# Kernel tuning notes

Hardware: AMD Instinct MI355X
Metric: run time of the kernel (lower is better)

The kernel has to match this reference:

```python
import jax, jax.numpy as jnp
import numpy as np

B, L = 1024, 1024
NCAT, NNUM = 20, 10
CAT_BUCKETS, SEQ_VOCAB = 100000, 50000
E, A, H, QH = 32, 128, 256, 256
TOPK = 30


def _init(key, shape, scale=0.02):
    return scale * jax.random.normal(key, shape, dtype=jnp.float32)


def setup_inputs() -> dict:
    key = jax.random.key(0)
    ks = jax.random.split(key, 24)
    z = lambda *s: jnp.zeros(s, dtype=jnp.float32)
    return {
        "cats": jax.random.randint(ks[0], (B, NCAT), 0, CAT_BUCKETS + 1),
        "nums": jax.random.normal(ks[1], (B, NNUM), dtype=jnp.float32),
        "seqs": jax.random.randint(ks[2], (B, L), 0, SEQ_VOCAB + 1),
        "tgt_ids": jax.random.randint(ks[3], (B,), 0, CAT_BUCKETS + 1),
        "cat_emb": _init(ks[4], (CAT_BUCKETS + 1, E)),
        "seq_emb": _init(ks[5], (SEQ_VOCAB + 1, E)),
        "Wnum": _init(ks[6], (NNUM, E)), "bnum": z(E),
        "Wq": _init(ks[7], (E, A)), "Wk": _init(ks[8], (E, A)), "Wv": _init(ks[9], (E, A)),
        "Wo": _init(ks[10], (A, E)), "bo": z(E),
        "Wpool": _init(ks[11], (NCAT * E, E)), "bpool": z(E),
        "Wmlp": _init(ks[12], (4 * E, H)), "bmlp": z(H),
        "q1_W1": _init(ks[13], (H, QH)), "q1_b1": z(QH),
        "q1_W2": _init(ks[14], (H, QH)), "q1_b2": z(QH),
        "q1_Wp": _init(ks[15], (QH, H)), "q1_bp": z(H),
        "q2_W1": _init(ks[16], (H, QH)), "q2_b1": z(QH),
        "q2_W2": _init(ks[17], (H, QH)), "q2_b2": z(QH),
        "q2_Wp": _init(ks[18], (QH, H)), "q2_bp": z(H),
        "Wout": _init(ks[19], (H, 1)), "bout": z(1),
    }


def _qnn(x, W1, b1, W2, b2, Wp, bp):
    # Quadratic neural block (QIN-style): Hadamard product of two linear maps,
    # projected back with a residual connection. Dropout is identity in eval.
    quad = (x @ W1 + b1) * (x @ W2 + b2)
    return x + quad @ Wp + bp


def reference(cats, nums, seqs, tgt_ids, cat_emb, seq_emb, Wnum, bnum, Wq, Wk, Wv,
              Wo, bo, Wpool, bpool, Wmlp, bmlp,
              q1_W1, q1_b1, q1_W2, q1_b2, q1_Wp, q1_bp,
              q2_W1, q2_b1, q2_W2, q2_b2, q2_Wp, q2_bp, Wout, bout):
    cat_e = cat_emb[cats]                                   # [B, NCAT, E]
    cat_pool = cat_e.reshape(cat_e.shape[0], -1) @ Wpool + bpool   # [B, E]
    num_e = nums @ Wnum + bnum                              # [B, E]
    tgt_e = cat_emb[tgt_ids]                                # [B, E] (tgt_emb shares cat_emb)
    seq_e = seq_emb[seqs]                                   # [B, L, E]

    q = tgt_e @ Wq                                          # [B, A]
    k = seq_e @ Wk                                          # [B, L, A]
    v = seq_e @ Wv                                          # [B, L, A]
    scores = jnp.einsum('ba,bla->bl', q, k) / jnp.sqrt(jnp.float32(A))

    # top-k + scatter mask + masked softmax == softmax over the top-k scores,
    # scattered implicitly via gather of the selected values.
    vals, idx = jax.lax.top_k(scores, TOPK)                 # [B, TOPK]
    w = jax.nn.softmax(vals, axis=1)                        # [B, TOPK]
    v_sel = jnp.take_along_axis(v, idx[:, :, None], axis=1)  # [B, TOPK, A]
    interest = jnp.einsum('bk,bka->ba', w, v_sel) @ Wo + bo  # [B, E]

    fused = jnp.concatenate([tgt_e, interest, cat_pool, num_e], axis=1)  # [B, 4E]
    h = jax.nn.relu(fused @ Wmlp + bmlp)                    # [B, H], dropout=eval
    h = _qnn(h, q1_W1, q1_b1, q1_W2, q1_b2, q1_Wp, q1_bp)
    h = _qnn(h, q2_W1, q2_b1, q2_W2, q2_b2, q2_Wp, q2_bp)
    return (h @ Wout + bout)[:, 0]                          # [B]
```

## Files before the change

kernel.cpp:

```cpp
#include <hip/hip_runtime.h>
#include <hip/hip_fp16.h>

#define B_ 1024
#define L_ 1024
#define NCAT_ 20
#define NNUM_ 10
#define E_ 32
#define A_ 128
#define H_ 256
#define TOPK_ 30
#define INV_SQRT_A 0.08838834764831845f

__device__ __forceinline__ void fma4(float4& a, float s, const float4 w) {
    a.x += s * w.x; a.y += s * w.y; a.z += s * w.z; a.w += s * w.w;
}
__device__ __forceinline__ float4 ldh4(const __half* p) {
    float2 rw = *(const float2*)p;
    const __half2* h = (const __half2*)&rw;
    float2 a = __half22float2(h[0]);
    float2 b = __half22float2(h[1]);
    return make_float4(a.x, a.y, b.x, b.y);
}
__device__ __forceinline__ void ldh24(const __half2* p, float4& w1, float4& w2) {
    float4 rw = *(const float4*)p;
    const __half2* h = (const __half2*)&rw;
    float2 f0 = __half22float2(h[0]), f1 = __half22float2(h[1]);
    float2 f2 = __half22float2(h[2]), f3 = __half22float2(h[3]);
    w1 = make_float4(f0.x, f1.x, f2.x, f3.x);
    w2 = make_float4(f0.y, f1.y, f2.y, f3.y);
}

#define K1_GRID 1356
__global__ __launch_bounds__(256) void fused_prep_kernel(
    const int* __restrict__ cats, const float* __restrict__ nums,
    const int* __restrict__ tgt_ids, const float* __restrict__ cat_emb,
    const float* __restrict__ Wnum, const float* __restrict__ bnum,
    const float* __restrict__ Wq, const float* __restrict__ Wk,
    const float* __restrict__ Wv, const float* __restrict__ Wo,
    const float* __restrict__ Wpool, const float* __restrict__ bpool,
    const float* __restrict__ seq_emb, const float* __restrict__ Wmlp,
    const float* __restrict__ q1W1, const float* __restrict__ q1W2,
    const float* __restrict__ q2W1, const float* __restrict__ q2W2,
    const float* __restrict__ q1Wp, const float* __restrict__ q2Wp,
    float* __restrict__ p_out, float* __restrict__ fused, float* __restrict__ M,
    __half2* __restrict__ seq_h2, __half2* __restrict__ Wmlp_h2,
    __half2* __restrict__ W12_1, __half2* __restrict__ W12_2,
    __half2* __restrict__ Wp1_h2, __half2* __restrict__ Wp2_h2)
{
    const int blk = blockIdx.x;
    const int t = threadIdx.x;

    if (blk < 256) {
        __shared__ float ce[4][NCAT_ * E_];
        __shared__ float tg[4][E_];
        __shared__ float nm[4][NNUM_];
        __shared__ float qs[4][A_];
        __shared__ float part[8][4][E_];
        const int r0 = blk * 4;

        for (int idx = t; idx < 640; idx += 256) {
            const int q = idx >> 3, f4 = idx & 7;
            const int row = q / 20, cat = q % 20;
            const int tok = cats[(r0 + row) * NCAT_ + cat];
            ((float4*)&ce[row][cat * 32])[f4] =
                ((const float4*)(cat_emb + (size_t)tok * 32))[f4];
        }
        if (t < 32) {
            const int row = t >> 3, f4 = t & 7;
            const int tok = tgt_ids[r0 + row];
            ((float4*)&tg[row][0])[f4] =
                ((const float4*)(cat_emb + (size_t)tok * 32))[f4];
        }
        if (t >= 64 && t < 104) {
            const int x = t - 64;
            nm[x / 10][x % 10] = nums[(r0 + x / 10) * NNUM_ + x % 10];
        }
        __syncthreads();

        {
            const int w = t >> 6, lane = t & 63;
            float q0 = 0.f, q1 = 0.f;
#pragma unroll
            for (int e = 0; e < E_; ++e) {
                float te = tg[w][e];
                q0 += te * Wq[e * A_ + lane];
                q1 += te * Wq[e * A_ + lane + 64];
            }
            qs[w][lane] = q0; qs[w][lane + 64] = q1;
        }

        {
            const int iseg = t >> 5;
            const int row = (t >> 3) & 3;
            const int c0 = (t & 7) * 4;
            float4 acc = make_float4(0.f, 0.f, 0.f, 0.f);
            const int i0 = iseg * 80;
            for (int i = i0; i < i0 + 80; ++i) {
                float4 wv = *(const float4*)(Wpool + i * 32 + c0);
                fma4(acc, ce[row][i], wv);
            }
            *(float4*)&part[iseg][row][c0] = acc;
        }
        __syncthreads();

        if (t < 128) {
            const int row = t >> 5, c = t & 31;
            const int b = r0 + row;
            float s = bpool[c];
#pragma unroll
            for (int g = 0; g < 8; ++g) s += part[g][row][c];
            fused[b * 128 + 64 + c] = s;
            fused[b * 128 + c] = tg[row][c];

            float ne = bnum[c];
#pragma unroll
            for (int n = 0; n < NNUM_; ++n) ne += nm[row][n] * Wnum[n * 32 + c];
            fused[b * 128 + 96 + c] = ne;

            float pv = 0.f;
#pragma unroll 8
            for (int a = 0; a < A_; ++a) pv += Wk[c * A_ + a] * qs[row][a];
            p_out[b * 32 + c] = pv;
        }
        return;
    }

    if (blk < 1280) {
        int x = (blk - 256) * 256 + t;
        for (; x < 800016; x += 1024 * 256) {
            float2 v = ((const float2*)seq_emb)[x];
            seq_h2[x] = __float22half2_rn(v);
        }
        return;
    }

    if (blk < 1284) {
        const int o = (blk - 1280) * 256 + t;
        const int j = o >> 5, e = o & 31;
        float sm = 0.f;
#pragma unroll 8
        for (int a = 0; a < A_; ++a) sm += Wv[j * A_ + a] * Wo[a * E_ + e];
        M[o] = sm;
        return;
    }

    if (blk < 1348) {
        int x = (blk - 1284) * 256 + t;
        for (; x < 65536; x += 64 * 256) {
            W12_1[x] = __float22half2_rn(make_float2(q1W1[x], q1W2[x]));
            W12_2[x] = __float22half2_rn(make_float2(q2W1[x], q2W2[x]));
        }
        return;
    }

    {
        int x = (blk - 1348) * 256 + t;
        for (; x < 16384; x += 8 * 256) {
            Wmlp_h2[x] = __float22half2_rn(((const float2*)Wmlp)[x]);
            Wp1_h2[x]  = __float22half2_rn(((const float2*)q1Wp)[x]);
            Wp2_h2[x]  = __float22half2_rn(((const float2*)q2Wp)[x]);
        }
    }
}

__global__ __launch_bounds__(512) void score_topk_kernel(
    const int* __restrict__ seqs, const __half* __restrict__ seq_h,
    const float* __restrict__ seq_emb, const float* __restrict__ p,
    const float* __restrict__ M, const float* __restrict__ bo,
    float* __restrict__ fused)
{
    const int b = blockIdx.x;
    const int t = threadIdx.x;

    __shared__ float sc[L_];
    __shared__ float ps[E_];
    __shared__ float sw[TOPK_];
    __shared__ int   stok[TOPK_];

    if (t < E_) ps[t] = p[b * E_ + t];
    __syncthreads();

    {
        const int tok1 = seqs[b * L_ + t];
        const int tok2 = seqs[b * L_ + t + 512];
        float4 buf[2][4];
        const float4* r1 = (const float4*)(seq_h + (size_t)tok1 * 32);
        const float4* r2 = (const float4*)(seq_h + (size_t)tok2 * 32);
#pragma unroll
        for (int i = 0; i < 4; ++i) buf[0][i] = r1[i];
#pragma unroll
        for (int i = 0; i < 4; ++i) buf[1][i] = r2[i];

        float acc0 = 0.f, acc1 = 0.f;
#pragma unroll
        for (int i = 0; i < 4; ++i) {
            const __half2* h1 = (const __half2*)&buf[0][i];
            const __half2* h2 = (const __half2*)&buf[1][i];
#pragma unroll
            for (int u = 0; u < 4; ++u) {
                float2 f1 = __half22float2(h1[u]);
                float2 f2 = __half22float2(h2[u]);
                acc0 += f1.x * ps[i * 8 + 2 * u] + f1.y * ps[i * 8 + 2 * u + 1];
                acc1 += f2.x * ps[i * 8 + 2 * u] + f2.y * ps[i * 8 + 2 * u + 1];
            }
        }
        sc[t] = acc0 * INV_SQRT_A;
        sc[t + 512] = acc1 * INV_SQRT_A;
    }
    __syncthreads();

    if (t >= 64) return;

    const int lane = t;
    float v[16];
#pragma unroll
    for (int j = 0; j < 16; ++j) v[j] = sc[j * 64 + lane];

    float lmax = v[0]; int lj = 0;
#pragma unroll
    for (int j = 1; j < 16; ++j) if (v[j] > lmax) { lmax = v[j]; lj = j; }

    float myv = -1e30f; int myl = 0;
    for (int k = 0; k < TOPK_; ++k) {
        float best = lmax; int bl = lj * 64 + lane;
#pragma unroll
        for (int off = 32; off > 0; off >>= 1) {
            float ov = __shfl_xor(best, off);
            int   ol = __shfl_xor(bl, off);
            if (ov > best || (ov == best && ol < bl)) { best = ov; bl = ol; }
        }
        if (lane == k) { myv = best; myl = bl; }
        if (lane == (bl & 63)) {
            v[bl >> 6] = -1e30f;
            lmax = v[0]; lj = 0;
#pragma unroll
            for (int j = 1; j < 16; ++j) if (v[j] > lmax) { lmax = v[j]; lj = j; }
        }
    }

    float m = myv;
#pragma unroll
    for (int off = 32; off > 0; off >>= 1) m = fmaxf(m, __shfl_xor(m, off));
    float e = (lane < TOPK_) ? expf(myv - m) : 0.f;
    float s = e;
#pragma unroll
    for (int off = 32; off > 0; off >>= 1) s += __shfl_xor(s, off);
    if (lane < TOPK_) {
        sw[lane]   = e / s;
        stok[lane] = seqs[b * L_ + myl];
    }

    if (lane < E_) {
        float acc = 0.f;
#pragma unroll
        for (int k = 0; k < TOPK_; ++k)
            acc += sw[k] * seq_emb[(size_t)stok[k] * 32 + lane];
        sc[lane] = acc;
    }
    if (lane < E_) {
        float acc = bo[lane];
#pragma unroll
        for (int j = 0; j < E_; ++j) acc += sc[j] * M[j * E_ + lane];
        fused[b * 128 + 32 + lane] = acc;
    }
}

#define RM 4
__global__ __launch_bounds__(512) void mlp_kernel(
    const float* __restrict__ fused,
    const __half* __restrict__ Wmlp_h, const float* __restrict__ bmlp,
    const __half2* __restrict__ W12_1, const float* __restrict__ b11,
    const float* __restrict__ b12, const __half* __restrict__ Wp1_h,
    const float* __restrict__ b1p,
    const __half2* __restrict__ W12_2, const float* __restrict__ b21,
    const float* __restrict__ b22, const __half* __restrict__ Wp2_h,
    const float* __restrict__ b2p,
    const float* __restrict__ Wout, const float* __restrict__ bout,
    float* __restrict__ out)
{
    const int b0 = blockIdx.x * RM;
    const int tid = threadIdx.x;
    const int cg = tid & 63;
    const int iseg = tid >> 6;
    const int c0 = cg * 4;

    __shared__ float xs[RM][128];
    __shared__ float hs[RM][H_];
    __shared__ float ts[RM][H_];
    __shared__ float part[2][8][RM][H_];
    __shared__ float red[8];

    for (int i = tid; i < RM * 128; i += 512) xs[i >> 7][i & 127] = fused[b0 * 128 + i];
    __syncthreads();

    {
        float4 acc[RM];
#pragma unroll
        for (int r = 0; r < RM; ++r) acc[r] = make_float4(0.f, 0.f, 0.f, 0.f);
        const int i0 = iseg * 16;
#pragma unroll
        for (int iq = 0; iq < 4; ++iq) {
            const int i = i0 + iq * 4;
            float4 w[4], xv[RM];
#pragma unroll
            for (int u = 0; u < 4; ++u) w[u] = ldh4(Wmlp_h + (i + u) * H_ + c0);
#pragma unroll
            for (int r = 0; r < RM; ++r) xv[r] = *(const float4*)(&xs[r][i]);
#pragma unroll
            for (int r = 0; r < RM; ++r) {
                fma4(acc[r], xv[r].x, w[0]); fma4(acc[r], xv[r].y, w[1]);
                fma4(acc[r], xv[r].z, w[2]); fma4(acc[r], xv[r].w, w[3]);
            }
        }
#pragma unroll
        for (int r = 0; r < RM; ++r) *(float4*)&part[0][iseg][r][c0] = acc[r];
    }
    __syncthreads();
    for (int o = tid; o < RM * H_; o += 512) {
        const int r = o >> 8, c = o & 255;
        float s = bmlp[c];
#pragma unroll
        for (int sg = 0; sg < 8; ++sg) s += part[0][sg][r][c];
        hs[r][c] = fmaxf(s, 0.f);
    }
    __syncthreads();

    const __half2* W12s[2] = { W12_1, W12_2 };
    const float* b1s[2] = { b11, b21 }; const float* b2s[2] = { b12, b22 };
    const __half* Wps[2] = { Wp1_h, Wp2_h }; const float* bps[2] = { b1p, b2p };

    for (int q = 0; q < 2; ++q) {
        const __half2* __restrict__ W12 = W12s[q];
        const __half*  __restrict__ Wp  = Wps[q];
        {
            float4 a1[RM], a2[RM];
#pragma unroll
            for (int r = 0; r < RM; ++r) {
                a1[r] = make_float4(0.f, 0.f, 0.f, 0.f);
                a2[r] = make_float4(0.f, 0.f, 0.f, 0.f);
            }
            const int i0 = iseg * 32;
#pragma unroll 2
            for (int iq = 0; iq < 8; ++iq) {
                const int i = i0 + iq * 4;
                float4 w1[4], w2[4], hv[RM];
#pragma unroll
                for (int u = 0; u < 4; ++u) ldh24(W12 + (i + u) * H_ + c0, w1[u], w2[u]);
#pragma unroll
                for (int r = 0; r < RM; ++r) hv[r] = *(const float4*)(&hs[r][i]);
#pragma unroll
                for (int r = 0; r < RM; ++r) {
                    fma4(a1[r], hv[r].x, w1[0]); fma4(a1[r], hv[r].y, w1[1]);
                    fma4(a1[r], hv[r].z, w1[2]); fma4(a1[r], hv[r].w, w1[3]);
                    fma4(a2[r], hv[r].x, w2[0]); fma4(a2[r], hv[r].y, w2[1]);
                    fma4(a2[r], hv[r].z, w2[2]); fma4(a2[r], hv[r].w, w2[3]);
                }
            }
#pragma unroll
            for (int r = 0; r < RM; ++r) {
                *(float4*)&part[0][iseg][r][c0] = a1[r];
                *(float4*)&part[1][iseg][r][c0] = a2[r];
            }
        }
        __syncthreads();
        {
            const float* b1 = b1s[q]; const float* b2 = b2s[q];
            for (int o = tid; o < RM * H_; o += 512) {
                const int r = o >> 8, c = o & 255;
                float t1 = b1[c], t2 = b2[c];
#pragma unroll
                for (int sg = 0; sg < 8; ++sg) { t1 += part[0][sg][r][c]; t2 += part[1][sg][r][c]; }
                ts[r][c] = t1 * t2;
            }
        }
        __syncthreads();
        {
            float4 ap[RM];
#pragma unroll
            for (int r = 0; r < RM; ++r) ap[r] = make_float4(0.f, 0.f, 0.f, 0.f);
            const int i0 = iseg * 32;
#pragma unroll 2
            for (int iq = 0; iq < 8; ++iq) {
                const int i = i0 + iq * 4;
                float4 w[4], tv[RM];
#pragma unroll
                for (int u = 0; u < 4; ++u) w[u] = ldh4(Wp + (i + u) * H_ + c0);
#pragma unroll
                for (int r = 0; r < RM; ++r) tv[r] = *(const float4*)(&ts[r][i]);
#pragma unroll
                for (int r = 0; r < RM; ++r) {
                    fma4(ap[r], tv[r].x, w[0]); fma4(ap[r], tv[r].y, w[1]);
                    fma4(ap[r], tv[r].z, w[2]); fma4(ap[r], tv[r].w, w[3]);
                }
            }
#pragma unroll
            for (int r = 0; r < RM; ++r) *(float4*)&part[0][iseg][r][c0] = ap[r];
        }
        __syncthreads();
        {
            const float* bp = bps[q];
            for (int o = tid; o < RM * H_; o += 512) {
                const int r = o >> 8, c = o & 255;
                float s = bp[c];
#pragma unroll
                for (int sg = 0; sg < 8; ++sg) s += part[0][sg][r][c];
                hs[r][c] += s;
            }
        }
        __syncthreads();
    }

    {
        const int r = tid >> 7, jj = tid & 127;
        float sum = hs[r][jj] * Wout[jj] + hs[r][jj + 128] * Wout[jj + 128];
#pragma unroll
        for (int off = 32; off > 0; off >>= 1) sum += __shfl_down(sum, off);
        if ((tid & 63) == 0) red[tid >> 6] = sum;
        __syncthreads();
        if (tid < RM) out[b0 + tid] = red[2 * tid] + red[2 * tid + 1] + bout[0];
    }
}

extern "C" void kernel_launch(void* const* d_in, const int* in_sizes, int n_in,
                              void* d_out, int out_size, void* d_ws, size_t ws_size,
                              hipStream_t stream) {
    const int*   cats    = (const int*)d_in[0];
    const float* nums    = (const float*)d_in[1];
    const int*   seqs    = (const int*)d_in[2];
    const int*   tgt_ids = (const int*)d_in[3];
    const float* cat_emb = (const float*)d_in[4];
    const float* seq_emb = (const float*)d_in[5];
    const float* Wnum    = (const float*)d_in[6];
    const float* bnum    = (const float*)d_in[7];
    const float* Wq      = (const float*)d_in[8];
    const float* Wk      = (const float*)d_in[9];
    const float* Wv      = (const float*)d_in[10];
    const float* Wo      = (const float*)d_in[11];
    const float* bo      = (const float*)d_in[12];
    const float* Wpool   = (const float*)d_in[13];
    const float* bpool   = (const float*)d_in[14];
    const float* Wmlp    = (const float*)d_in[15];
    const float* bmlp    = (const float*)d_in[16];
    const float* q1_W1   = (const float*)d_in[17];
    const float* q1_b1   = (const float*)d_in[18];
    const float* q1_W2   = (const float*)d_in[19];
    const float* q1_b2   = (const float*)d_in[20];
    const float* q1_Wp   = (const float*)d_in[21];
    const float* q1_bp   = (const float*)d_in[22];
    const float* q2_W1   = (const float*)d_in[23];
    const float* q2_b1   = (const float*)d_in[24];
    const float* q2_W2   = (const float*)d_in[25];
    const float* q2_b2   = (const float*)d_in[26];
    const float* q2_Wp   = (const float*)d_in[27];
    const float* q2_bp   = (const float*)d_in[28];
    const float* Wout    = (const float*)d_in[29];
    const float* bout    = (const float*)d_in[30];

    float* ws = (float*)d_ws;
    float*   p       = ws;
    float*   fused   = ws + 32768;
    float*   M       = ws + 163840;
    __half2* seq_h2  = (__half2*)(ws + 164864);
    __half2* Wmlp_h2 = (__half2*)(ws + 964928);
    __half2* W12_1   = (__half2*)(ws + 981312);
    __half2* W12_2   = (__half2*)(ws + 1046848);
    __half2* Wp1_h2  = (__half2*)(ws + 1112384);
    __half2* Wp2_h2  = (__half2*)(ws + 1128768);

    float* out = (float*)d_out;

    fused_prep_kernel<<<K1_GRID, 256, 0, stream>>>(
        cats, nums, tgt_ids, cat_emb, Wnum, bnum, Wq, Wk, Wv, Wo,
        Wpool, bpool, seq_emb, Wmlp,
        q1_W1, q1_W2, q2_W1, q2_W2, q1_Wp, q2_Wp,
        p, fused, M, seq_h2, Wmlp_h2, W12_1, W12_2, Wp1_h2, Wp2_h2);

    score_topk_kernel<<<B_, 512, 0, stream>>>(
        seqs, (const __half*)seq_h2, seq_emb, p, M, bo, fused);

    mlp_kernel<<<B_ / RM, 512, 0, stream>>>(
        fused, (const __half*)Wmlp_h2, bmlp,
        W12_1, q1_b1, q1_b2, (const __half*)Wp1_h2, q1_bp,
        W12_2, q2_b1, q2_b2, (const __half*)Wp2_h2, q2_bp,
        Wout, bout, out);
}
```

Measured before the change: 195.0 us.

## Fuse score/top-k attention into the MLP kernel, four rows per block

Merges the per-row score/top-k kernel into the MLP kernel, so each 512-thread block computes scores and top-k for four batch rows and then runs the MLP on them. The interest vector goes straight into shared memory instead of round-tripping through the global fused buffer, and one kernel launch is removed. The cost is far fewer blocks for the score phase (256 instead of 1024), more shared memory per block and lower occupancy, which may hurt latency hiding on the gather-heavy score phase.

```diff
diff --git a/kernel.cpp b/kernel.cpp
--- a/kernel.cpp
+++ b/kernel.cpp
@@ -163,110 +163,11 @@
     }
 }
 
-__global__ __launch_bounds__(512) void score_topk_kernel(
+#define RM 4
+__global__ __launch_bounds__(512) void score_mlp_kernel(
     const int* __restrict__ seqs, const __half* __restrict__ seq_h,
     const float* __restrict__ seq_emb, const float* __restrict__ p,
     const float* __restrict__ M, const float* __restrict__ bo,
-    float* __restrict__ fused)
-{
-    const int b = blockIdx.x;
-    const int t = threadIdx.x;
-
-    __shared__ float sc[L_];
-    __shared__ float ps[E_];
-    __shared__ float sw[TOPK_];
-    __shared__ int   stok[TOPK_];
-
-    if (t < E_) ps[t] = p[b * E_ + t];
-    __syncthreads();
-
-    {
-        const int tok1 = seqs[b * L_ + t];
-        const int tok2 = seqs[b * L_ + t + 512];
-        float4 buf[2][4];
-        const float4* r1 = (const float4*)(seq_h + (size_t)tok1 * 32);
-        const float4* r2 = (const float4*)(seq_h + (size_t)tok2 * 32);
-#pragma unroll
-        for (int i = 0; i < 4; ++i) buf[0][i] = r1[i];
-#pragma unroll
-        for (int i = 0; i < 4; ++i) buf[1][i] = r2[i];
-
-        float acc0 = 0.f, acc1 = 0.f;
-#pragma unroll
-        for (int i = 0; i < 4; ++i) {
-            const __half2* h1 = (const __half2*)&buf[0][i];
-            const __half2* h2 = (const __half2*)&buf[1][i];
-#pragma unroll
-            for (int u = 0; u < 4; ++u) {
-                float2 f1 = __half22float2(h1[u]);
-                float2 f2 = __half22float2(h2[u]);
-                acc0 += f1.x * ps[i * 8 + 2 * u] + f1.y * ps[i * 8 + 2 * u + 1];
-                acc1 += f2.x * ps[i * 8 + 2 * u] + f2.y * ps[i * 8 + 2 * u + 1];
-            }
-        }
-        sc[t] = acc0 * INV_SQRT_A;
-        sc[t + 512] = acc1 * INV_SQRT_A;
-    }
-    __syncthreads();
-
-    if (t >= 64) return;
-
-    const int lane = t;
-    float v[16];
-#pragma unroll
-    for (int j = 0; j < 16; ++j) v[j] = sc[j * 64 + lane];
-
-    float lmax = v[0]; int lj = 0;
-#pragma unroll
-    for (int j = 1; j < 16; ++j) if (v[j] > lmax) { lmax = v[j]; lj = j; }
-
-    float myv = -1e30f; int myl = 0;
-    for (int k = 0; k < TOPK_; ++k) {
-        float best = lmax; int bl = lj * 64 + lane;
-#pragma unroll
-        for (int off = 32; off > 0; off >>= 1) {
-            float ov = __shfl_xor(best, off);
-            int   ol = __shfl_xor(bl, off);
-            if (ov > best || (ov == best && ol < bl)) { best = ov; bl = ol; }
-        }
-        if (lane == k) { myv = best; myl = bl; }
-        if (lane == (bl & 63)) {
-            v[bl >> 6] = -1e30f;
-            lmax = v[0]; lj = 0;
-#pragma unroll
-            for (int j = 1; j < 16; ++j) if (v[j] > lmax) { lmax = v[j]; lj = j; }
-        }
-    }
-
-    float m = myv;
-#pragma unroll
-    for (int off = 32; off > 0; off >>= 1) m = fmaxf(m, __shfl_xor(m, off));
-    float e = (lane < TOPK_) ? expf(myv - m) : 0.f;
-    float s = e;
-#pragma unroll
-    for (int off = 32; off > 0; off >>= 1) s += __shfl_xor(s, off);
-    if (lane < TOPK_) {
-        sw[lane]   = e / s;
-        stok[lane] = seqs[b * L_ + myl];
-    }
-
-    if (lane < E_) {
-        float acc = 0.f;
-#pragma unroll
-        for (int k = 0; k < TOPK_; ++k)
-            acc += sw[k] * seq_emb[(size_t)stok[k] * 32 + lane];
-        sc[lane] = acc;
-    }
-    if (lane < E_) {
-        float acc = bo[lane];
-#pragma unroll
-        for (int j = 0; j < E_; ++j) acc += sc[j] * M[j * E_ + lane];
-        fused[b * 128 + 32 + lane] = acc;
-    }
-}
-
-#define RM 4
-__global__ __launch_bounds__(512) void mlp_kernel(
     const float* __restrict__ fused,
     const __half* __restrict__ Wmlp_h, const float* __restrict__ bmlp,
     const __half2* __restrict__ W12_1, const float* __restrict__ b11,
@@ -280,18 +181,124 @@
 {
     const int b0 = blockIdx.x * RM;
     const int tid = threadIdx.x;
-    const int cg = tid & 63;
-    const int iseg = tid >> 6;
-    const int c0 = cg * 4;
-
+
+    __shared__ float sc[RM][L_];
+    __shared__ float ps[RM][E_];
+    __shared__ float sw[RM][32];
+    __shared__ int   stok[RM][32];
     __shared__ float xs[RM][128];
     __shared__ float hs[RM][H_];
     __shared__ float ts[RM][H_];
     __shared__ float part[2][8][RM][H_];
     __shared__ float red[8];
 
-    for (int i = tid; i < RM * 128; i += 512) xs[i >> 7][i & 127] = fused[b0 * 128 + i];
+    if (tid < 128) ps[tid >> 5][tid & 31] = p[(b0 + (tid >> 5)) * 32 + (tid & 31)];
     __syncthreads();
+
+    {
+        const int row = tid >> 7;
+        const int s = tid & 127;
+        const int bb = b0 + row;
+#pragma unroll
+        for (int jj = 0; jj < 4; ++jj) {
+            const int l1 = jj * 256 + s;
+            const int l2 = l1 + 128;
+            const int tok1 = seqs[bb * L_ + l1];
+            const int tok2 = seqs[bb * L_ + l2];
+            float4 buf[2][4];
+            const float4* r1 = (const float4*)(seq_h + (size_t)tok1 * 32);
+            const float4* r2 = (const float4*)(seq_h + (size_t)tok2 * 32);
+#pragma unroll
+            for (int i = 0; i < 4; ++i) buf[0][i] = r1[i];
+#pragma unroll
+            for (int i = 0; i < 4; ++i) buf[1][i] = r2[i];
+
+            float acc0 = 0.f, acc1 = 0.f;
+#pragma unroll
+            for (int i = 0; i < 4; ++i) {
+                const __half2* h1 = (const __half2*)&buf[0][i];
+                const __half2* h2 = (const __half2*)&buf[1][i];
+#pragma unroll
+                for (int u = 0; u < 4; ++u) {
+                    float2 f1 = __half22float2(h1[u]);
+                    float2 f2 = __half22float2(h2[u]);
+                    acc0 += f1.x * ps[row][i * 8 + 2 * u] + f1.y * ps[row][i * 8 + 2 * u + 1];
+                    acc1 += f2.x * ps[row][i * 8 + 2 * u] + f2.y * ps[row][i * 8 + 2 * u + 1];
+                }
+            }
+            sc[row][l1] = acc0 * INV_SQRT_A;
+            sc[row][l2] = acc1 * INV_SQRT_A;
+        }
+    }
+    if (tid < 384) {
+        const int r = tid / 96, c0 = tid % 96;
+        const int c = (c0 < 32) ? c0 : (c0 + 32);
+        xs[r][c] = fused[(b0 + r) * 128 + c];
+    }
+    __syncthreads();
+
+    if (tid < 256) {
+        const int w = tid >> 6;
+        const int lane = tid & 63;
+        const int bb = b0 + w;
+
+        float v[16];
+#pragma unroll
+        for (int j = 0; j < 16; ++j) v[j] = sc[w][j * 64 + lane];
+
+        float lmax = v[0]; int lj = 0;
+#pragma unroll
+        for (int j = 1; j < 16; ++j) if (v[j] > lmax) { lmax = v[j]; lj = j; }
+
+        float myv = -1e30f; int myl = 0;
+        for (int k = 0; k < TOPK_; ++k) {
+            float best = lmax; int bl = lj * 64 + lane;
+#pragma unroll
+            for (int off = 32; off > 0; off >>= 1) {
+                float ov = __shfl_xor(best, off);
+                int   ol = __shfl_xor(bl, off);
+                if (ov > best || (ov == best && ol < bl)) { best = ov; bl = ol; }
+            }
+            if (lane == k) { myv = best; myl = bl; }
+            if (lane == (bl & 63)) {
+                v[bl >> 6] = -1e30f;
+                lmax = v[0]; lj = 0;
+#pragma unroll
+                for (int j = 1; j < 16; ++j) if (v[j] > lmax) { lmax = v[j]; lj = j; }
+            }
+        }
+
+        float m = myv;
+#pragma unroll
+        for (int off = 32; off > 0; off >>= 1) m = fmaxf(m, __shfl_xor(m, off));
+        float e = (lane < TOPK_) ? expf(myv - m) : 0.f;
+        float s = e;
+#pragma unroll
+        for (int off = 32; off > 0; off >>= 1) s += __shfl_xor(s, off);
+        if (lane < TOPK_) {
+            sw[w][lane]   = e / s;
+            stok[w][lane] = seqs[bb * L_ + myl];
+        }
+
+        if (lane < E_) {
+            float acc = 0.f;
+#pragma unroll
+            for (int k = 0; k < TOPK_; ++k)
+                acc += sw[w][k] * seq_emb[(size_t)stok[w][k] * 32 + lane];
+            sc[w][lane] = acc;
+        }
+        if (lane < E_) {
+            float acc = bo[lane];
+#pragma unroll
+            for (int j = 0; j < E_; ++j) acc += sc[w][j] * M[j * E_ + lane];
+            xs[w][32 + lane] = acc;
+        }
+    }
+    __syncthreads();
+
+    const int cg = tid & 63;
+    const int iseg = tid >> 6;
+    const int c0 = cg * 4;
 
     {
         float4 acc[RM];
@@ -475,11 +482,9 @@
         q1_W1, q1_W2, q2_W1, q2_W2, q1_Wp, q2_Wp,
         p, fused, M, seq_h2, Wmlp_h2, W12_1, W12_2, Wp1_h2, Wp2_h2);
 
-    score_topk_kernel<<<B_, 512, 0, stream>>>(
-        seqs, (const __half*)seq_h2, seq_emb, p, M, bo, fused);
-
-    mlp_kernel<<<B_ / RM, 512, 0, stream>>>(
-        fused, (const __half*)Wmlp_h2, bmlp,
+    score_mlp_kernel<<<B_ / RM, 512, 0, stream>>>(
+        seqs, (const __half*)seq_h2, seq_emb, p, M, bo, fused,
+        (const __half*)Wmlp_h2, bmlp,
         W12_1, q1_b1, q1_b2, (const __half*)Wp1_h2, q1_bp,
         W12_2, q2_b1, q2_b2, (const __half*)Wp2_h2, q2_bp,
         Wout, bout, out);
```

Measured after the change: 194.4 us. Within noise of the previous version (-0.3%).
